# Performance work log

Measured on AMD Instinct MI355X. Metric: run time of the kernel, lower is better.

## Reference

```python
import jax, jax.numpy as jnp
import numpy as np

N_NODES = 50000
N_EDGES = 800000
IN_DIM = 64
HID = 128
NUM_GRAPHS = 256


def setup_inputs() -> dict:
    key = jax.random.key(0)
    ks = jax.random.split(key, 20)
    inp = {
        'x': jax.random.normal(ks[0], (N_NODES, IN_DIM), dtype=jnp.float32),
        'edge_index': jax.random.randint(ks[1], (2, N_EDGES), 0, N_NODES, dtype=jnp.int32),
        'batch_idx': jnp.sort(jax.random.randint(ks[2], (N_NODES,), 0, NUM_GRAPHS, dtype=jnp.int32)),
    }
    # GIN layer MLP params (3 layers): Linear(in,hid)->ReLU->Linear(hid,hid)
    dims = [(IN_DIM, HID), (HID, HID), (HID, HID)]
    ki = 3
    for li, (di, dh) in enumerate(dims):
        s1 = 1.0 / np.sqrt(di)
        s2 = 1.0 / np.sqrt(dh)
        inp[f'gin{li}_w1'] = jax.random.uniform(ks[ki], (di, dh), jnp.float32, -s1, s1); ki += 1
        inp[f'gin{li}_b1'] = jnp.zeros((dh,), jnp.float32)
        inp[f'gin{li}_w2'] = jax.random.uniform(ks[ki], (dh, dh), jnp.float32, -s2, s2); ki += 1
        inp[f'gin{li}_b2'] = jnp.zeros((dh,), jnp.float32)
    # head: Linear(2*HID, HID) -> ReLU -> (Dropout eval=id) -> Linear(HID, 1)
    sh = 1.0 / np.sqrt(2 * HID)
    so = 1.0 / np.sqrt(HID)
    inp['head_w1'] = jax.random.uniform(ks[ki], (2 * HID, HID), jnp.float32, -sh, sh); ki += 1
    inp['head_b1'] = jnp.zeros((HID,), jnp.float32)
    inp['head_w2'] = jax.random.uniform(ks[ki], (HID, 1), jnp.float32, -so, so); ki += 1
    inp['head_b2'] = jnp.zeros((1,), jnp.float32)
    return inp


def _gin_layer(h, src, dst, w1, b1, w2, b2):
    # GINConv with eps=0: mlp(x + sum_{j->i} x_j), followed by outer ReLU
    agg = jax.ops.segment_sum(h[src], dst, num_segments=N_NODES)
    z = h + agg
    z = jnp.dot(jax.nn.relu(jnp.dot(z, w1) + b1), w2) + b2
    return jax.nn.relu(z)


def reference(x, edge_index, batch_idx,
              gin0_w1, gin0_b1, gin0_w2, gin0_b2,
              gin1_w1, gin1_b1, gin1_w2, gin1_b2,
              gin2_w1, gin2_b1, gin2_w2, gin2_b2,
              head_w1, head_b1, head_w2, head_b2):
    src, dst = edge_index[0], edge_index[1]
    h = _gin_layer(x, src, dst, gin0_w1, gin0_b1, gin0_w2, gin0_b2)
    h = _gin_layer(h, src, dst, gin1_w1, gin1_b1, gin1_w2, gin1_b2)
    h = _gin_layer(h, src, dst, gin2_w1, gin2_b1, gin2_w2, gin2_b2)
    # meanmax readout over graphs
    cnt = jax.ops.segment_sum(jnp.ones((h.shape[0],), h.dtype), batch_idx,
                              num_segments=NUM_GRAPHS)  # [G]
    ssum = jax.ops.segment_sum(h, batch_idx, num_segments=NUM_GRAPHS)  # [G, HID]
    mean_pool = ssum / jnp.maximum(cnt, 1.0)[:, None]
    max_pool = jax.ops.segment_max(h, batch_idx, num_segments=NUM_GRAPHS)
    max_pool = jnp.where(cnt[:, None] > 0, max_pool, 0.0)
    graph_repr = jnp.concatenate([mean_pool, max_pool], axis=-1)  # [G, 2*HID]
    # fraud head (dropout is identity in eval)
    hh = jax.nn.relu(jnp.dot(graph_repr, head_w1) + head_b1)
    logits = jnp.dot(hh, head_w2) + head_b2  # [G, 1]
    score = jax.nn.sigmoid(logits)
    return score
```

## Files before the change

### kernel.cpp

```cpp
#include <hip/hip_runtime.h>
#include <hip/hip_bf16.h>

#define N_NODES   50000
#define N_EDGES   800000
#define IN_DIM    64
#define HID       128
#define NUM_GRAPHS 256
#define NBUCK     196
#define BCAP      8192

typedef __bf16 bf16x8 __attribute__((ext_vector_type(8)));
typedef unsigned short u16x8 __attribute__((ext_vector_type(8)));
typedef float f32x4 __attribute__((ext_vector_type(4)));

__device__ __forceinline__ float b2f(unsigned short u) {
    return __uint_as_float(((unsigned int)u) << 16);
}
__device__ __forceinline__ unsigned short f2b(float f) {
    unsigned int x = __float_as_uint(f);
    x = (x + 0x7fffu + ((x >> 16) & 1u)) >> 16;
    return (unsigned short)x;
}

__global__ void diag_kernel(unsigned short* out, unsigned short pat) {
    out[threadIdx.x] = pat;
}

__global__ __launch_bounds__(256) void mega_pre_kernel(
    const unsigned short* __restrict__ x,
    const void* w0, const void* w1, const void* w2,
    const void* w3, const void* w4, const void* w5,
    unsigned short* __restrict__ wfbase,
    const int* __restrict__ batch, int* __restrict__ gstart,
    float* __restrict__ psum, unsigned int* __restrict__ pmax,
    const void* hw1, unsigned short* __restrict__ w1t,
    int* __restrict__ bcursor, int* __restrict__ flagp) {
    int b = blockIdx.x;
    int tid = threadIdx.x;

    if (b < 352) {
        __shared__ int cnt;
        if (tid == 0) cnt = 0;
        __syncthreads();
        unsigned short u = x[2 * tid];
        int e = (u >> 7) & 0xff;
        if (e <= 100 || e >= 140) atomicAdd(&cnt, 1);
        __syncthreads();
        int flag = cnt > 64;

        int mat, boff;
        if (b < 32) { mat = 0; boff = b; }
        else { mat = 1 + (b - 32) / 64; boff = (b - 32) % 64; }
        const void* W = mat == 0 ? w0 : mat == 1 ? w1 : mat == 2 ? w2
                      : mat == 3 ? w3 : mat == 4 ? w4 : w5;
        int KC = (mat == 0) ? 2 : 4;
        int idx = boff * 256 + tid;
        int j  = idx & 7;
        int l  = (idx >> 3) & 63;
        int tc = idx >> 9;
        int c  = tc % KC;
        int t  = tc / KC;
        int k  = c * 32 + (l >> 4) * 8 + j;
        int n  = t * 16 + (l & 15);
        unsigned short v = flag ? f2b(((const float*)W)[k * 128 + n])
                                : ((const unsigned short*)W)[k * 128 + n];
        wfbase[mat * 16384 + idx] = v;
    } else if (b < 548) {
        int i = (b - 352) * 256 + tid;
        if (i < NUM_GRAPHS * HID) { psum[i] = 0.0f; pmax[i] = 0u; }
        if (i >= N_NODES) return;
        int b1 = batch[i];
        int b0 = (i == 0) ? -1 : batch[i - 1];
        for (int g = b0 + 1; g <= b1; g++) gstart[g] = i;
        if (i == N_NODES - 1)
            for (int g = b1 + 1; g <= NUM_GRAPHS; g++) gstart[g] = N_NODES;
    } else if (b < 580) {
        __shared__ int cnt;
        if (tid == 0) cnt = 0;
        __syncthreads();
        unsigned short u = x[2 * tid];
        int e = (u >> 7) & 0xff;
        if (e <= 100 || e >= 140) atomicAdd(&cnt, 1);
        __syncthreads();
        int flag = cnt > 64;
        int base = (b - 548) * 1024;
#pragma unroll
        for (int j = 0; j < 4; j++) {
            int idx = base + j * 256 + tid;
            int n = idx >> 8;
            int k = idx & 255;
            unsigned short v = flag ? f2b(((const float*)hw1)[k * 128 + n])
                                    : ((const unsigned short*)hw1)[k * 128 + n];
            w1t[idx] = v;
        }
    } else {
        if (tid < NBUCK) bcursor[tid] = tid * BCAP;
        __shared__ int cnt;
        if (tid == 0) cnt = 0;
        __syncthreads();
        int c = 0;
        for (int j = 0; j < 16; j++) {
            unsigned short u = x[2 * (tid * 16 + j)];
            int e = (u >> 7) & 0xff;
            if (e <= 100 || e >= 140) c++;
        }
        atomicAdd(&cnt, c);
        __syncthreads();
        if (tid == 0) *flagp = (cnt > 1024) ? 1 : 0;
    }
}

__global__ __launch_bounds__(1024) void bscatter_kernel(const int* __restrict__ src,
        const int* __restrict__ dst, int* __restrict__ bcursor,
        unsigned int* __restrict__ ebuf) {
    __shared__ int lcnt[NBUCK];
    __shared__ int lbase[NBUCK];
    __shared__ int lcur[NBUCK];
    int tid = threadIdx.x;
    if (tid < NBUCK) lcnt[tid] = 0;
    __syncthreads();
    int e0 = blockIdx.x * 4096;
    int d[4], s[4];
#pragma unroll
    for (int k = 0; k < 4; k++) {
        int e = e0 + k * 1024 + tid;
        if (e < N_EDGES) {
            d[k] = dst[e]; s[k] = src[e];
            atomicAdd(&lcnt[d[k] >> 8], 1);
        } else d[k] = -1;
    }
    __syncthreads();
    if (tid < NBUCK) {
        int c = lcnt[tid];
        lbase[tid] = c ? atomicAdd(&bcursor[tid], c) : 0;
        lcur[tid] = 0;
    }
    __syncthreads();
#pragma unroll
    for (int k = 0; k < 4; k++) {
        if (d[k] >= 0) {
            int b = d[k] >> 8;
            int p = lbase[b] + atomicAdd(&lcur[b], 1);
            ebuf[p] = ((unsigned int)(d[k] & 255) << 16) | (unsigned int)s[k];
        }
    }
}

__global__ __launch_bounds__(256) void bsort_kernel(const unsigned int* __restrict__ ebuf,
        const int* __restrict__ bcursor, int* __restrict__ off,
        unsigned short* __restrict__ csr) {
    __shared__ int cntA[256];
    __shared__ int sc[256];
    __shared__ int lcnt[256];
    __shared__ int lcur[256];
    int b = blockIdx.x, tid = threadIdx.x;

    int v = (tid < NBUCK) ? (bcursor[tid] - tid * BCAP) : 0;
    cntA[tid] = v;
    sc[tid] = v;
    __syncthreads();
    for (int d = 1; d < 256; d <<= 1) {
        int t = (tid >= d) ? sc[tid - d] : 0;
        __syncthreads();
        sc[tid] += t;
        __syncthreads();
    }
    int base = sc[b] - cntA[b];
    int cnt  = cntA[b];
    int ebase = b * BCAP;
    __syncthreads();

    lcnt[tid] = 0;
    __syncthreads();
    for (int i = tid; i < cnt; i += 256)
        atomicAdd(&lcnt[ebuf[ebase + i] >> 16], 1);
    __syncthreads();
    int v2 = lcnt[tid];
    sc[tid] = v2;
    __syncthreads();
    for (int d = 1; d < 256; d <<= 1) {
        int t = (tid >= d) ? sc[tid - d] : 0;
        __syncthreads();
        sc[tid] += t;
        __syncthreads();
    }
    int excl = sc[tid] - v2;
    lcur[tid] = excl;
    int node = b * 256 + tid;
    if (node < N_NODES) off[node] = base + excl;
    if (b == 0 && tid == 0) off[N_NODES] = N_EDGES;
    __syncthreads();
    for (int i = tid; i < cnt; i += 256) {
        unsigned int ev = ebuf[ebase + i];
        int p = atomicAdd(&lcur[ev >> 16], 1);
        csr[base + p] = (unsigned short)(ev & 0xffffu);
    }
}

__global__ __launch_bounds__(256) void gather_x_kernel(const void* __restrict__ x,
        const int* __restrict__ off, const unsigned short* __restrict__ csr,
        unsigned short* __restrict__ z, const int* __restrict__ flagp) {
    int flag = *flagp;
    int wave = threadIdx.x >> 6;
    int lane = threadIdx.x & 63;
    int node = blockIdx.x * 16 + wave * 4 + (lane >> 4);
    int l = lane & 15;
    int s = off[node], e = off[node + 1];
    float a0, a1, a2, a3;
    float b0 = 0.f, b1 = 0.f, b2 = 0.f, b3 = 0.f;
    float c0 = 0.f, c1 = 0.f, c2 = 0.f, c3 = 0.f;
    float d0 = 0.f, d1 = 0.f, d2 = 0.f, d3 = 0.f;
    if (flag) {
        const float4* xp = (const float4*)x;
        float4 u = xp[(size_t)node * 16 + l];
        a0 = u.x; a1 = u.y; a2 = u.z; a3 = u.w;
        int i = s;
        for (; i + 3 < e; i += 4) {
            float4 v0 = xp[(size_t)csr[i] * 16 + l];
            float4 v1 = xp[(size_t)csr[i + 1] * 16 + l];
            float4 v2 = xp[(size_t)csr[i + 2] * 16 + l];
            float4 v3 = xp[(size_t)csr[i + 3] * 16 + l];
            a0 += v0.x; a1 += v0.y; a2 += v0.z; a3 += v0.w;
            b0 += v1.x; b1 += v1.y; b2 += v1.z; b3 += v1.w;
            c0 += v2.x; c1 += v2.y; c2 += v2.z; c3 += v2.w;
            d0 += v3.x; d1 += v3.y; d2 += v3.z; d3 += v3.w;
        }
        for (; i < e; i++) {
            float4 v = xp[(size_t)csr[i] * 16 + l];
            a0 += v.x; a1 += v.y; a2 += v.z; a3 += v.w;
        }
    } else {
        const ushort4* xp = (const ushort4*)x;
        ushort4 u = xp[(size_t)node * 16 + l];
        a0 = b2f(u.x); a1 = b2f(u.y); a2 = b2f(u.z); a3 = b2f(u.w);
        int i = s;
        for (; i + 3 < e; i += 4) {
            ushort4 v0 = xp[(size_t)csr[i] * 16 + l];
            ushort4 v1 = xp[(size_t)csr[i + 1] * 16 + l];
            ushort4 v2 = xp[(size_t)csr[i + 2] * 16 + l];
            ushort4 v3 = xp[(size_t)csr[i + 3] * 16 + l];
            a0 += b2f(v0.x); a1 += b2f(v0.y); a2 += b2f(v0.z); a3 += b2f(v0.w);
            b0 += b2f(v1.x); b1 += b2f(v1.y); b2 += b2f(v1.z); b3 += b2f(v1.w);
            c0 += b2f(v2.x); c1 += b2f(v2.y); c2 += b2f(v2.z); c3 += b2f(v2.w);
            d0 += b2f(v3.x); d1 += b2f(v3.y); d2 += b2f(v3.z); d3 += b2f(v3.w);
        }
        for (; i < e; i++) {
            ushort4 v = xp[(size_t)csr[i] * 16 + l];
            a0 += b2f(v.x); a1 += b2f(v.y); a2 += b2f(v.z); a3 += b2f(v.w);
        }
    }
    ushort4 o;
    o.x = f2b(a0 + b0 + c0 + d0);
    o.y = f2b(a1 + b1 + c1 + d1);
    o.z = f2b(a2 + b2 + c2 + d2);
    o.w = f2b(a3 + b3 + c3 + d3);
    ((ushort4*)z)[(size_t)node * 16 + l] = o;
}

__global__ __launch_bounds__(256) void gather128_kernel(const unsigned short* __restrict__ h,
        const int* __restrict__ off, const unsigned short* __restrict__ csr,
        unsigned short* __restrict__ z) {
    int wave = threadIdx.x >> 6;
    int lane = threadIdx.x & 63;
    int node = blockIdx.x * 16 + wave * 4 + (lane >> 4);
    int l = lane & 15;
    int s = off[node], e = off[node + 1];
    const u16x8* hp = (const u16x8*)h;
    u16x8 u = hp[(size_t)node * 16 + l];
    float a[8], b[8], c[8], d[8];
#pragma unroll
    for (int j = 0; j < 8; j++) { a[j] = b2f(u[j]); b[j] = 0.f; c[j] = 0.f; d[j] = 0.f; }
    int i = s;
    for (; i + 3 < e; i += 4) {
        u16x8 v0 = hp[(size_t)csr[i] * 16 + l];
        u16x8 v1 = hp[(size_t)csr[i + 1] * 16 + l];
        u16x8 v2 = hp[(size_t)csr[i + 2] * 16 + l];
        u16x8 v3 = hp[(size_t)csr[i + 3] * 16 + l];
#pragma unroll
        for (int j = 0; j < 8; j++) {
            a[j] += b2f(v0[j]); b[j] += b2f(v1[j]);
            c[j] += b2f(v2[j]); d[j] += b2f(v3[j]);
        }
    }
    for (; i < e; i++) {
        u16x8 v = hp[(size_t)csr[i] * 16 + l];
#pragma unroll
        for (int j = 0; j < 8; j++) a[j] += b2f(v[j]);
    }
    u16x8 o;
#pragma unroll
    for (int j = 0; j < 8; j++) o[j] = f2b(a[j] + b[j] + c[j] + d[j]);
    ((u16x8*)z)[(size_t)node * 16 + l] = o;
}

template <int K1, bool POOL>
__global__ __launch_bounds__(256, 3) void gin_mlp_kernel(
    const unsigned short* __restrict__ Z,
    const unsigned short* __restrict__ Wf1, const void* __restrict__ bias1,
    const unsigned short* __restrict__ Wf2, const void* __restrict__ bias2,
    unsigned short* __restrict__ Out, int M, const int* __restrict__ flagp,
    const int* __restrict__ batch, float* __restrict__ psum,
    unsigned int* __restrict__ pmax) {
    constexpr int KC1 = K1 / 32;
    __shared__ unsigned short lds_hi[64 * 136];
    __shared__ unsigned short lds_lo[64 * 136];
    __shared__ int batch_lds[64];

    int flag = *flagp;
    int wave = threadIdx.x >> 6;
    int lane = threadIdx.x & 63;
    int m_ = lane & 15;
    int q  = lane >> 4;
    int rowbase = blockIdx.x * 64 + wave * 16;
    int row  = rowbase + m_;
    int rowc = row < M ? row : (M - 1);

    if constexpr (POOL) {
        if (threadIdx.x < 64) {
            int gr = blockIdx.x * 64 + threadIdx.x;
            batch_lds[threadIdx.x] = gr < M ? batch[gr] : -1;
        }
    }

    const unsigned short* zrow = Z + (size_t)rowc * K1 + q * 8;
    const unsigned short* wfl1 = Wf1 + lane * 8;
    const unsigned short* wfl2 = Wf2 + lane * 8;

    bf16x8 afrag[KC1];
#pragma unroll
    for (int c = 0; c < KC1; c++)
        afrag[c] = *reinterpret_cast<const bf16x8*>(zrow + c * 32);

    float b1v[8], b2v[8];
#pragma unroll
    for (int t = 0; t < 8; t++) {
        int col = t * 16 + m_;
        b1v[t] = flag ? ((const float*)bias1)[col]
                      : b2f(((const unsigned short*)bias1)[col]);
        b2v[t] = flag ? ((const float*)bias2)[col]
                      : b2f(((const unsigned short*)bias2)[col]);
    }

    f32x4 acc[8];
#pragma unroll
    for (int t = 0; t < 8; t++) acc[t] = (f32x4)(0.0f);

    {
        bf16x8 wb[8], wn[8];
#pragma unroll
        for (int t = 0; t < 8; t++)
            wb[t] = *reinterpret_cast<const bf16x8*>(wfl1 + ((t * KC1 + 0) << 9));
#pragma unroll
        for (int c = 0; c < KC1; c++) {
            if (c + 1 < KC1) {
#pragma unroll
                for (int t = 0; t < 8; t++)
                    wn[t] = *reinterpret_cast<const bf16x8*>(wfl1 + ((t * KC1 + c + 1) << 9));
            }
#pragma unroll
            for (int t = 0; t < 8; t++)
                acc[t] = __builtin_amdgcn_mfma_f32_16x16x32_bf16(afrag[c], wb[t], acc[t], 0, 0, 0);
            if (c + 1 < KC1) {
#pragma unroll
                for (int t = 0; t < 8; t++) wb[t] = wn[t];
            }
        }
    }

#pragma unroll
    for (int r = 0; r < 4; r++) {
        int lr = wave * 16 + q * 4 + r;
#pragma unroll
        for (int t = 0; t < 8; t++) {
            int col = t * 16 + m_;
            float v = acc[t][r] + b1v[t];
            v = v > 0.0f ? v : 0.0f;
            unsigned short hb = f2b(v);
            lds_hi[lr * 136 + col] = hb;
            lds_lo[lr * 136 + col] = f2b(v - b2f(hb));
        }
    }

#pragma unroll
    for (int t = 0; t < 8; t++) acc[t] = (f32x4)(0.0f);

    {
        int lr2 = wave * 16 + m_;
        const unsigned short* hibase = &lds_hi[lr2 * 136 + q * 8];
        const unsigned short* lobase = &lds_lo[lr2 * 136 + q * 8];
        bf16x8 wb[8], wn[8];
#pragma unroll
        for (int t = 0; t < 8; t++)
            wb[t] = *reinterpret_cast<const bf16x8*>(wfl2 + ((t * 4 + 0) << 9));
#pragma unroll
        for (int c = 0; c < 4; c++) {
            if (c < 3) {
#pragma unroll
                for (int t = 0; t < 8; t++)
                    wn[t] = *reinterpret_cast<const bf16x8*>(wfl2 + ((t * 4 + c + 1) << 9));
            }
            bf16x8 ahi = *reinterpret_cast<const bf16x8*>(hibase + c * 32);
            bf16x8 alo = *reinterpret_cast<const bf16x8*>(lobase + c * 32);
#pragma unroll
            for (int t = 0; t < 8; t++) {
                acc[t] = __builtin_amdgcn_mfma_f32_16x16x32_bf16(ahi, wb[t], acc[t], 0, 0, 0);
                acc[t] = __builtin_amdgcn_mfma_f32_16x16x32_bf16(alo, wb[t], acc[t], 0, 0, 0);
            }
            if (c < 3) {
#pragma unroll
                for (int t = 0; t < 8; t++) wb[t] = wn[t];
            }
        }
    }

#pragma unroll
    for (int r = 0; r < 4; r++) {
        int lr = wave * 16 + q * 4 + r;
        int orow = blockIdx.x * 64 + lr;
#pragma unroll
        for (int t = 0; t < 8; t++) {
            int col = t * 16 + m_;
            float v = acc[t][r] + b2v[t];
            v = v > 0.0f ? v : 0.0f;
            if constexpr (POOL) {
                lds_hi[lr * 136 + col] = f2b(v);
            } else {
                if (orow < M) Out[(size_t)orow * HID + col] = f2b(v);
            }
        }
    }

    if constexpr (POOL) {
        __syncthreads();
        int f = threadIdx.x;
        if (f < HID) {
            int cur = -1;
            float sum = 0.0f, mx = 0.0f;
            for (int rrow = 0; rrow < 64; rrow++) {
                int g = batch_lds[rrow];
                if (g < 0) break;
                float v = b2f(lds_hi[rrow * 136 + f]);
                if (g == cur) {
                    sum += v;
                    mx = fmaxf(mx, v);
                } else {
                    if (cur >= 0) {
                        atomicAdd(&psum[cur * HID + f], sum);
                        atomicMax(&pmax[cur * HID + f], __float_as_uint(mx));
                    }
                    cur = g; sum = v; mx = v;
                }
            }
            if (cur >= 0) {
                atomicAdd(&psum[cur * HID + f], sum);
                atomicMax(&pmax[cur * HID + f], __float_as_uint(mx));
            }
        }
    }
}

__global__ __launch_bounds__(128) void head_kernel(
    const float* __restrict__ psum, const unsigned int* __restrict__ pmax,
    const int* __restrict__ gstart,
    const unsigned short* __restrict__ w1t,
    const void* __restrict__ b1, const void* __restrict__ w2,
    const void* __restrict__ b2,
    void* __restrict__ out, const int* __restrict__ flagp) {
    int g = blockIdx.x;
    int n = threadIdx.x;
    int flag = *flagp;
    __shared__ float repr[2 * HID];
    __shared__ float red[HID];

    float c = (float)(gstart[g + 1] - gstart[g]);
    float inv = 1.0f / fmaxf(c, 1.0f);
    repr[n]       = psum[g * HID + n] * inv;
    repr[HID + n] = __uint_as_float(pmax[g * HID + n]);
    __syncthreads();

    const u16x8* wp = (const u16x8*)(w1t + n * 256);
    float a0 = 0.f, a1 = 0.f, a2 = 0.f, a3 = 0.f;
#pragma unroll
    for (int c8 = 0; c8 < 32; c8 += 4) {
        u16x8 w0 = wp[c8 + 0];
        u16x8 w1 = wp[c8 + 1];
        u16x8 w2v = wp[c8 + 2];
        u16x8 w3 = wp[c8 + 3];
#pragma unroll
        for (int j = 0; j < 8; j++) {
            a0 += repr[(c8 + 0) * 8 + j] * b2f(w0[j]);
            a1 += repr[(c8 + 1) * 8 + j] * b2f(w1[j]);
            a2 += repr[(c8 + 2) * 8 + j] * b2f(w2v[j]);
            a3 += repr[(c8 + 3) * 8 + j] * b2f(w3[j]);
        }
    }
    float b1v = flag ? ((const float*)b1)[n] : b2f(((const unsigned short*)b1)[n]);
    float acc = a0 + a1 + a2 + a3 + b1v;
    acc = fmaxf(acc, 0.0f);

    float w2s = flag ? ((const float*)w2)[n] : b2f(((const unsigned short*)w2)[n]);
    red[n] = acc * w2s;
    __syncthreads();
    for (int s = 64; s > 0; s >>= 1) {
        if (n < s) red[n] += red[n + s];
        __syncthreads();
    }
    if (n == 0) {
        float b2v = flag ? ((const float*)b2)[0] : b2f(((const unsigned short*)b2)[0]);
        float logit = red[0] + b2v;
        float sv = 1.0f / (1.0f + expf(-logit));
        if (flag) ((float*)out)[g] = sv;
        else      ((unsigned short*)out)[g] = f2b(sv);
    }
}

extern "C" void kernel_launch(void* const* d_in, const int* in_sizes, int n_in,
                              void* d_out, int out_size, void* d_ws, size_t ws_size,
                              hipStream_t stream) {
    const int* edge = (const int*)d_in[1];
    const int* srcv = edge;
    const int* dstv = edge + N_EDGES;
    const int* batch = (const int*)d_in[2];

    char* ws = (char*)d_ws;
    unsigned short* A = (unsigned short*)ws;
    unsigned short* B = (unsigned short*)(ws + 12800000);
    unsigned int* ebuf = (unsigned int*)(ws + 25600000);
    unsigned short* csr = (unsigned short*)(ws + 32100000);
    int* off    = (int*)(ws + 33700000);
    unsigned short* wfbase = (unsigned short*)(ws + 33904000);
    float* psum  = (float*)(ws + 34100608);
    unsigned int* pmax = (unsigned int*)(ws + 34231680);
    int* bcursor = (int*)(ws + 34362752);
    int* gstart  = (int*)(ws + 34363776);
    int* flagp   = (int*)(ws + 34365824);
    unsigned short* w1t = (unsigned short*)(ws + 34366848);

    const size_t NEED = 34500000;
    if (ws_size < NEED) {
        unsigned int k = 0;
        while ((((size_t)1) << (k + 1)) <= ws_size && k < 62) k++;
        diag_kernel<<<1, 256, 0, stream>>>((unsigned short*)d_out,
                                           (unsigned short)(0x4000 | (k & 63)));
        return;
    }

    mega_pre_kernel<<<581, 256, 0, stream>>>(
        (const unsigned short*)d_in[0],
        d_in[3], d_in[5], d_in[7], d_in[9], d_in[11], d_in[13], wfbase,
        batch, gstart, psum, pmax, d_in[15], w1t, bcursor, flagp);

    const int EB = (N_EDGES + 4095) / 4096;
    bscatter_kernel<<<EB, 1024, 0, stream>>>(srcv, dstv, bcursor, ebuf);
    bsort_kernel<<<NBUCK, 256, 0, stream>>>(ebuf, bcursor, off, csr);

    const int GEMM_GRID = (N_NODES + 63) / 64;
    const int GATHER_GRID = N_NODES / 16;

    gather_x_kernel<<<GATHER_GRID, 256, 0, stream>>>(d_in[0], off, csr, B, flagp);
    gin_mlp_kernel<64, false><<<GEMM_GRID, 256, 0, stream>>>(
        B, wfbase + 0 * 16384, d_in[4], wfbase + 1 * 16384, d_in[6],
        A, N_NODES, flagp, batch, psum, pmax);

    gather128_kernel<<<GATHER_GRID, 256, 0, stream>>>(A, off, csr, B);
    gin_mlp_kernel<128, false><<<GEMM_GRID, 256, 0, stream>>>(
        B, wfbase + 2 * 16384, d_in[8], wfbase + 3 * 16384, d_in[10],
        A, N_NODES, flagp, batch, psum, pmax);

    gather128_kernel<<<GATHER_GRID, 256, 0, stream>>>(A, off, csr, B);
    gin_mlp_kernel<128, true><<<GEMM_GRID, 256, 0, stream>>>(
        B, wfbase + 4 * 16384, d_in[12], wfbase + 5 * 16384, d_in[14],
        A , N_NODES, flagp, batch, psum, pmax);

    head_kernel<<<NUM_GRAPHS, 128, 0, stream>>>(psum, pmax, gstart, w1t,
                                                d_in[16], d_in[17], d_in[18],
                                                d_out, flagp);
}
```

Before: 268.8 us.

## Fuse neighbor gather into GIN MLP kernel via LDS staging

Merges the separate gather kernels into the per-layer MLP kernel. Each 64-row block now aggregates its own nodes' neighbor features, writes the bf16 sums into LDS, and reads the A fragments from LDS rather than from a global intermediate. This removes the global write and read of the aggregated tensor and three kernel launches per forward. In exchange, the gather runs inside a kernel bounded by launch_bounds occupancy, 4 nodes per wave per pass, which may hide gather latency less well. Ping-pong buffers now alternate A and B.

```diff
diff --git a/kernel.cpp b/kernel.cpp
--- a/kernel.cpp
+++ b/kernel.cpp
@@ -197,113 +197,18 @@
     }
 }
 
-__global__ __launch_bounds__(256) void gather_x_kernel(const void* __restrict__ x,
-        const int* __restrict__ off, const unsigned short* __restrict__ csr,
-        unsigned short* __restrict__ z, const int* __restrict__ flagp) {
-    int flag = *flagp;
-    int wave = threadIdx.x >> 6;
-    int lane = threadIdx.x & 63;
-    int node = blockIdx.x * 16 + wave * 4 + (lane >> 4);
-    int l = lane & 15;
-    int s = off[node], e = off[node + 1];
-    float a0, a1, a2, a3;
-    float b0 = 0.f, b1 = 0.f, b2 = 0.f, b3 = 0.f;
-    float c0 = 0.f, c1 = 0.f, c2 = 0.f, c3 = 0.f;
-    float d0 = 0.f, d1 = 0.f, d2 = 0.f, d3 = 0.f;
-    if (flag) {
-        const float4* xp = (const float4*)x;
-        float4 u = xp[(size_t)node * 16 + l];
-        a0 = u.x; a1 = u.y; a2 = u.z; a3 = u.w;
-        int i = s;
-        for (; i + 3 < e; i += 4) {
-            float4 v0 = xp[(size_t)csr[i] * 16 + l];
-            float4 v1 = xp[(size_t)csr[i + 1] * 16 + l];
-            float4 v2 = xp[(size_t)csr[i + 2] * 16 + l];
-            float4 v3 = xp[(size_t)csr[i + 3] * 16 + l];
-            a0 += v0.x; a1 += v0.y; a2 += v0.z; a3 += v0.w;
-            b0 += v1.x; b1 += v1.y; b2 += v1.z; b3 += v1.w;
-            c0 += v2.x; c1 += v2.y; c2 += v2.z; c3 += v2.w;
-            d0 += v3.x; d1 += v3.y; d2 += v3.z; d3 += v3.w;
-        }
-        for (; i < e; i++) {
-            float4 v = xp[(size_t)csr[i] * 16 + l];
-            a0 += v.x; a1 += v.y; a2 += v.z; a3 += v.w;
-        }
-    } else {
-        const ushort4* xp = (const ushort4*)x;
-        ushort4 u = xp[(size_t)node * 16 + l];
-        a0 = b2f(u.x); a1 = b2f(u.y); a2 = b2f(u.z); a3 = b2f(u.w);
-        int i = s;
-        for (; i + 3 < e; i += 4) {
-            ushort4 v0 = xp[(size_t)csr[i] * 16 + l];
-            ushort4 v1 = xp[(size_t)csr[i + 1] * 16 + l];
-            ushort4 v2 = xp[(size_t)csr[i + 2] * 16 + l];
-            ushort4 v3 = xp[(size_t)csr[i + 3] * 16 + l];
-            a0 += b2f(v0.x); a1 += b2f(v0.y); a2 += b2f(v0.z); a3 += b2f(v0.w);
-            b0 += b2f(v1.x); b1 += b2f(v1.y); b2 += b2f(v1.z); b3 += b2f(v1.w);
-            c0 += b2f(v2.x); c1 += b2f(v2.y); c2 += b2f(v2.z); c3 += b2f(v2.w);
-            d0 += b2f(v3.x); d1 += b2f(v3.y); d2 += b2f(v3.z); d3 += b2f(v3.w);
-        }
-        for (; i < e; i++) {
-            ushort4 v = xp[(size_t)csr[i] * 16 + l];
-            a0 += b2f(v.x); a1 += b2f(v.y); a2 += b2f(v.z); a3 += b2f(v.w);
-        }
-    }
-    ushort4 o;
-    o.x = f2b(a0 + b0 + c0 + d0);
-    o.y = f2b(a1 + b1 + c1 + d1);
-    o.z = f2b(a2 + b2 + c2 + d2);
-    o.w = f2b(a3 + b3 + c3 + d3);
-    ((ushort4*)z)[(size_t)node * 16 + l] = o;
-}
-
-__global__ __launch_bounds__(256) void gather128_kernel(const unsigned short* __restrict__ h,
-        const int* __restrict__ off, const unsigned short* __restrict__ csr,
-        unsigned short* __restrict__ z) {
-    int wave = threadIdx.x >> 6;
-    int lane = threadIdx.x & 63;
-    int node = blockIdx.x * 16 + wave * 4 + (lane >> 4);
-    int l = lane & 15;
-    int s = off[node], e = off[node + 1];
-    const u16x8* hp = (const u16x8*)h;
-    u16x8 u = hp[(size_t)node * 16 + l];
-    float a[8], b[8], c[8], d[8];
-#pragma unroll
-    for (int j = 0; j < 8; j++) { a[j] = b2f(u[j]); b[j] = 0.f; c[j] = 0.f; d[j] = 0.f; }
-    int i = s;
-    for (; i + 3 < e; i += 4) {
-        u16x8 v0 = hp[(size_t)csr[i] * 16 + l];
-        u16x8 v1 = hp[(size_t)csr[i + 1] * 16 + l];
-        u16x8 v2 = hp[(size_t)csr[i + 2] * 16 + l];
-        u16x8 v3 = hp[(size_t)csr[i + 3] * 16 + l];
-#pragma unroll
-        for (int j = 0; j < 8; j++) {
-            a[j] += b2f(v0[j]); b[j] += b2f(v1[j]);
-            c[j] += b2f(v2[j]); d[j] += b2f(v3[j]);
-        }
-    }
-    for (; i < e; i++) {
-        u16x8 v = hp[(size_t)csr[i] * 16 + l];
-#pragma unroll
-        for (int j = 0; j < 8; j++) a[j] += b2f(v[j]);
-    }
-    u16x8 o;
-#pragma unroll
-    for (int j = 0; j < 8; j++) o[j] = f2b(a[j] + b[j] + c[j] + d[j]);
-    ((u16x8*)z)[(size_t)node * 16 + l] = o;
-}
-
-template <int K1, bool POOL>
-__global__ __launch_bounds__(256, 3) void gin_mlp_kernel(
-    const unsigned short* __restrict__ Z,
+template <int K1, bool POOL, bool FROMX>
+__global__ __launch_bounds__(256, 3) void fused_gin_kernel(
+    const void* __restrict__ X,
+    const int* __restrict__ off, const unsigned short* __restrict__ csr,
     const unsigned short* __restrict__ Wf1, const void* __restrict__ bias1,
     const unsigned short* __restrict__ Wf2, const void* __restrict__ bias2,
     unsigned short* __restrict__ Out, int M, const int* __restrict__ flagp,
     const int* __restrict__ batch, float* __restrict__ psum,
     unsigned int* __restrict__ pmax) {
     constexpr int KC1 = K1 / 32;
-    __shared__ unsigned short lds_hi[64 * 136];
-    __shared__ unsigned short lds_lo[64 * 136];
+    __shared__ __align__(16) unsigned short lds_hi[64 * 136];
+    __shared__ __align__(16) unsigned short lds_lo[64 * 136];
     __shared__ int batch_lds[64];
 
     int flag = *flagp;
@@ -311,9 +216,6 @@
     int lane = threadIdx.x & 63;
     int m_ = lane & 15;
     int q  = lane >> 4;
-    int rowbase = blockIdx.x * 64 + wave * 16;
-    int row  = rowbase + m_;
-    int rowc = row < M ? row : (M - 1);
 
     if constexpr (POOL) {
         if (threadIdx.x < 64) {
@@ -322,14 +224,102 @@
         }
     }
 
-    const unsigned short* zrow = Z + (size_t)rowc * K1 + q * 8;
+    int np = lane >> 4;
+    int l  = lane & 15;
+#pragma unroll 1
+    for (int p = 0; p < 4; p++) {
+        int nl = wave * 16 + p * 4 + np;
+        int node = blockIdx.x * 64 + nl;
+        int nodec = node < M ? node : (M - 1);
+        int s = off[nodec], e = off[nodec + 1];
+        if constexpr (FROMX) {
+            float a0, a1, a2, a3;
+            float b0 = 0.f, b1 = 0.f, b2 = 0.f, b3 = 0.f;
+            float c0 = 0.f, c1 = 0.f, c2 = 0.f, c3 = 0.f;
+            float d0 = 0.f, d1 = 0.f, d2 = 0.f, d3 = 0.f;
+            if (flag) {
+                const float4* xp = (const float4*)X;
+                float4 u = xp[(size_t)nodec * 16 + l];
+                a0 = u.x; a1 = u.y; a2 = u.z; a3 = u.w;
+                int i = s;
+                for (; i + 3 < e; i += 4) {
+                    float4 v0 = xp[(size_t)csr[i] * 16 + l];
+                    float4 v1 = xp[(size_t)csr[i + 1] * 16 + l];
+                    float4 v2 = xp[(size_t)csr[i + 2] * 16 + l];
+                    float4 v3 = xp[(size_t)csr[i + 3] * 16 + l];
+                    a0 += v0.x; a1 += v0.y; a2 += v0.z; a3 += v0.w;
+                    b0 += v1.x; b1 += v1.y; b2 += v1.z; b3 += v1.w;
+                    c0 += v2.x; c1 += v2.y; c2 += v2.z; c3 += v2.w;
+                    d0 += v3.x; d1 += v3.y; d2 += v3.z; d3 += v3.w;
+                }
+                for (; i < e; i++) {
+                    float4 v = xp[(size_t)csr[i] * 16 + l];
+                    a0 += v.x; a1 += v.y; a2 += v.z; a3 += v.w;
+                }
+            } else {
+                const ushort4* xp = (const ushort4*)X;
+                ushort4 u = xp[(size_t)nodec * 16 + l];
+                a0 = b2f(u.x); a1 = b2f(u.y); a2 = b2f(u.z); a3 = b2f(u.w);
+                int i = s;
+                for (; i + 3 < e; i += 4) {
+                    ushort4 v0 = xp[(size_t)csr[i] * 16 + l];
+                    ushort4 v1 = xp[(size_t)csr[i + 1] * 16 + l];
+                    ushort4 v2 = xp[(size_t)csr[i + 2] * 16 + l];
+                    ushort4 v3 = xp[(size_t)csr[i + 3] * 16 + l];
+                    a0 += b2f(v0.x); a1 += b2f(v0.y); a2 += b2f(v0.z); a3 += b2f(v0.w);
+                    b0 += b2f(v1.x); b1 += b2f(v1.y); b2 += b2f(v1.z); b3 += b2f(v1.w);
+                    c0 += b2f(v2.x); c1 += b2f(v2.y); c2 += b2f(v2.z); c3 += b2f(v2.w);
+                    d0 += b2f(v3.x); d1 += b2f(v3.y); d2 += b2f(v3.z); d3 += b2f(v3.w);
+                }
+                for (; i < e; i++) {
+                    ushort4 v = xp[(size_t)csr[i] * 16 + l];
+                    a0 += b2f(v.x); a1 += b2f(v.y); a2 += b2f(v.z); a3 += b2f(v.w);
+                }
+            }
+            ushort4 o;
+            o.x = f2b(a0 + b0 + c0 + d0);
+            o.y = f2b(a1 + b1 + c1 + d1);
+            o.z = f2b(a2 + b2 + c2 + d2);
+            o.w = f2b(a3 + b3 + c3 + d3);
+            *reinterpret_cast<ushort4*>(&lds_hi[nl * 136 + l * 4]) = o;
+        } else {
+            const u16x8* hp = (const u16x8*)X;
+            u16x8 u = hp[(size_t)nodec * 16 + l];
+            float a[8], b[8], c[8], d[8];
+#pragma unroll
+            for (int j = 0; j < 8; j++) { a[j] = b2f(u[j]); b[j] = 0.f; c[j] = 0.f; d[j] = 0.f; }
+            int i = s;
+            for (; i + 3 < e; i += 4) {
+                u16x8 v0 = hp[(size_t)csr[i] * 16 + l];
+                u16x8 v1 = hp[(size_t)csr[i + 1] * 16 + l];
+                u16x8 v2 = hp[(size_t)csr[i + 2] * 16 + l];
+                u16x8 v3 = hp[(size_t)csr[i + 3] * 16 + l];
+#pragma unroll
+                for (int j = 0; j < 8; j++) {
+                    a[j] += b2f(v0[j]); b[j] += b2f(v1[j]);
+                    c[j] += b2f(v2[j]); d[j] += b2f(v3[j]);
+                }
+            }
+            for (; i < e; i++) {
+                u16x8 v = hp[(size_t)csr[i] * 16 + l];
+#pragma unroll
+                for (int j = 0; j < 8; j++) a[j] += b2f(v[j]);
+            }
+            u16x8 o;
+#pragma unroll
+            for (int j = 0; j < 8; j++) o[j] = f2b(a[j] + b[j] + c[j] + d[j]);
+            *reinterpret_cast<u16x8*>(&lds_hi[nl * 136 + l * 8]) = o;
+        }
+    }
+
     const unsigned short* wfl1 = Wf1 + lane * 8;
     const unsigned short* wfl2 = Wf2 + lane * 8;
+    const unsigned short* zlds = &lds_hi[(wave * 16 + m_) * 136 + q * 8];
 
     bf16x8 afrag[KC1];
 #pragma unroll
     for (int c = 0; c < KC1; c++)
-        afrag[c] = *reinterpret_cast<const bf16x8*>(zrow + c * 32);
+        afrag[c] = *reinterpret_cast<const bf16x8*>(zlds + c * 32);
 
     float b1v[8], b2v[8];
 #pragma unroll
@@ -555,21 +545,20 @@
     bsort_kernel<<<NBUCK, 256, 0, stream>>>(ebuf, bcursor, off, csr);
 
     const int GEMM_GRID = (N_NODES + 63) / 64;
-    const int GATHER_GRID = N_NODES / 16;
-
-    gather_x_kernel<<<GATHER_GRID, 256, 0, stream>>>(d_in[0], off, csr, B, flagp);
-    gin_mlp_kernel<64, false><<<GEMM_GRID, 256, 0, stream>>>(
-        B, wfbase + 0 * 16384, d_in[4], wfbase + 1 * 16384, d_in[6],
+
+    fused_gin_kernel<64, false, true><<<GEMM_GRID, 256, 0, stream>>>(
+        d_in[0], off, csr,
+        wfbase + 0 * 16384, d_in[4], wfbase + 1 * 16384, d_in[6],
         A, N_NODES, flagp, batch, psum, pmax);
 
-    gather128_kernel<<<GATHER_GRID, 256, 0, stream>>>(A, off, csr, B);
-    gin_mlp_kernel<128, false><<<GEMM_GRID, 256, 0, stream>>>(
-        B, wfbase + 2 * 16384, d_in[8], wfbase + 3 * 16384, d_in[10],
-        A, N_NODES, flagp, batch, psum, pmax);
-
-    gather128_kernel<<<GATHER_GRID, 256, 0, stream>>>(A, off, csr, B);
-    gin_mlp_kernel<128, true><<<GEMM_GRID, 256, 0, stream>>>(
-        B, wfbase + 4 * 16384, d_in[12], wfbase + 5 * 16384, d_in[14],
+    fused_gin_kernel<128, false, false><<<GEMM_GRID, 256, 0, stream>>>(
+        A, off, csr,
+        wfbase + 2 * 16384, d_in[8], wfbase + 3 * 16384, d_in[10],
+        B, N_NODES, flagp, batch, psum, pmax);
+
+    fused_gin_kernel<128, true, false><<<GEMM_GRID, 256, 0, stream>>>(
+        B, off, csr,
+        wfbase + 4 * 16384, d_in[12], wfbase + 5 * 16384, d_in[14],
         A , N_NODES, flagp, batch, psum, pmax);
 
     head_kernel<<<NUM_GRAPHS, 128, 0, stream>>>(psum, pmax, gstart, w1t,
```

Result: faster. 254.7 us (-5.3%).
